# Optimization experiments

Measured on AMD Instinct MI355X. Metric: run time of the kernel, lower is better.

Reference implementation:

```python
import jax, jax.numpy as jnp
import numpy as np

N_NODES = 100000
N_EDGES = 3200000
NUM_FEATURES = 5
HIDDEN = 64


def _gcn_layer(x, W, b, src, dst, norm, n_nodes):
    """One GCNConv: out = scatter_add(norm * (xW)[src] -> dst) + b.
    src/dst/norm already include self-loops and symmetric normalization."""
    h = x @ W                                  # [N, out_ch] small dense GEMM
    msg = h[src] * norm[:, None]               # [E+N, out_ch] gather + scale
    out = jax.ops.segment_sum(msg, dst, num_segments=n_nodes)
    return out + b


def _build_norm(edge_index, n_nodes):
    """Add self-loops, compute D^{-1/2}[src] * D^{-1/2}[dst] (GCN symmetric norm)."""
    loop = jnp.arange(n_nodes, dtype=edge_index.dtype)
    src = jnp.concatenate([edge_index[0], loop])
    dst = jnp.concatenate([edge_index[1], loop])
    deg = jax.ops.segment_sum(jnp.ones_like(dst, dtype=jnp.float32), dst,
                              num_segments=n_nodes)
    dis = jnp.where(deg > 0, jax.lax.rsqrt(deg), 0.0)  # deg^{-1/2}
    norm = dis[src] * dis[dst]
    return src, dst, norm


def setup_inputs() -> dict:
    key = jax.random.key(0)
    ks = jax.random.split(key, 8)
    x = jax.random.normal(ks[0], (N_NODES, NUM_FEATURES), dtype=jnp.float32)
    edge_index = jax.random.randint(ks[1], (2, N_EDGES), 0, N_NODES, dtype=jnp.int64)
    # glorot-ish scaled params
    W1 = jax.random.normal(ks[2], (NUM_FEATURES, HIDDEN), dtype=jnp.float32) * (1.0 / np.sqrt(NUM_FEATURES))
    b1 = jnp.zeros((HIDDEN,), dtype=jnp.float32)
    W2 = jax.random.normal(ks[3], (HIDDEN, HIDDEN), dtype=jnp.float32) * (1.0 / np.sqrt(HIDDEN))
    b2 = jnp.zeros((HIDDEN,), dtype=jnp.float32)
    W3 = jax.random.normal(ks[4], (HIDDEN, 1), dtype=jnp.float32) * (1.0 / np.sqrt(HIDDEN))
    b3 = jnp.zeros((1,), dtype=jnp.float32)
    return {"x": x, "edge_index": edge_index,
            "W1": W1, "b1": b1, "W2": W2, "b2": b2, "W3": W3, "b3": b3}


def reference(x, edge_index, W1, b1, W2, b2, W3, b3):
    n_nodes = x.shape[0]
    src, dst, norm = _build_norm(edge_index, n_nodes)
    h = jax.nn.relu(_gcn_layer(x, W1, b1, src, dst, norm, n_nodes))
    h = jax.nn.relu(_gcn_layer(h, W2, b2, src, dst, norm, n_nodes))
    out = _gcn_layer(h, W3, b3, src, dst, norm, n_nodes)  # [N, 1]
    return out
```

## Files before the change

kernel.cpp:

```cpp
#include <hip/hip_runtime.h>
#include <hip/hip_fp16.h>

#define NFEAT 5
#define HID 64
#define BSH 9
#define BNODES 512
#define MAXBK 256
#define CHUNK 4096
#define ECAPMAX 20480

__global__ void k_binit(int* bcur, int ecap) {
    bcur[threadIdx.x] = threadIdx.x * ecap;
}

__global__ __launch_bounds__(256) void
k_bin(const int* __restrict__ src, const int* __restrict__ dst,
      int* bcur, unsigned* __restrict__ binned, int E) {
    __shared__ unsigned stg[CHUNK];
    __shared__ unsigned char bkt[CHUNK];
    __shared__ int hist[MAXBK], base[MAXBK], gb[MAXBK];
    int t = threadIdx.x;
    int e0 = blockIdx.x * CHUNK;
    int cc = E - e0; if (cc > CHUNK) cc = CHUNK;
    hist[t] = 0;
    __syncthreads();
    unsigned me[CHUNK / 256]; int mb[CHUNK / 256]; int mr[CHUNK / 256];
#pragma unroll
    for (int k = 0; k < CHUNK / 256; ++k) {
        int i = e0 + k * 256 + t;
        if (i < E) {
            int s = src[i], d = dst[i];
            mb[k] = d >> BSH;
            me[k] = (unsigned)s | ((unsigned)(d & (BNODES - 1)) << 17);
            mr[k] = atomicAdd(&hist[mb[k]], 1);
        } else mb[k] = -1;
    }
    __syncthreads();
    int c = hist[t];
    base[t] = c;
    __syncthreads();
    for (int off = 1; off < 256; off <<= 1) {
        int a = (t >= off) ? base[t - off] : 0;
        __syncthreads();
        base[t] += a;
        __syncthreads();
    }
    base[t] -= c;
    gb[t] = c ? atomicAdd(&bcur[t], c) : 0;
    __syncthreads();
#pragma unroll
    for (int k = 0; k < CHUNK / 256; ++k)
        if (mb[k] >= 0) {
            int p = base[mb[k]] + mr[k];
            stg[p] = me[k];
            bkt[p] = (unsigned char)mb[k];
        }
    __syncthreads();
#pragma unroll
    for (int k = 0; k < CHUNK / 256; ++k) {
        int p = k * 256 + t;
        if (p < cc) {
            int b = bkt[p];
            binned[gb[b] + (p - base[b])] = stg[p];
        }
    }
}

__global__ __launch_bounds__(256) void
k_sort(const unsigned* __restrict__ binned, const int* __restrict__ bcur,
       const float* __restrict__ x, int* __restrict__ rpN, int* __restrict__ rpE,
       int* __restrict__ csr, float* __restrict__ dis, float* __restrict__ xs,
       int n, int ecap) {
    __shared__ unsigned short rank[ECAPMAX];
    __shared__ int hist[BNODES];
    __shared__ int cur[BNODES];
    __shared__ int tmp[256];
    int t = threadIdx.x, b = blockIdx.x;
    int e0 = b * ecap;
    int cnt = bcur[b] - e0;
    if (cnt > ecap) cnt = ecap;
    int v0 = b << BSH;
    int nv = n - v0; if (nv > BNODES) nv = BNODES;
    hist[t] = 0; hist[t + 256] = 0;
    __syncthreads();
    for (int i = t; i < cnt; i += 256) {
        int vl = binned[e0 + i] >> 17;
        rank[i] = (unsigned short)atomicAdd(&hist[vl], 1);
    }
    __syncthreads();
    for (int vl = t; vl < nv; vl += 256) {
        int v = v0 + vl;
        float dv = rsqrtf((float)hist[vl] + 1.0f);
        dis[v] = dv;
        const float* xr = x + (size_t)v * NFEAT;
        float* xw = xs + (size_t)v * 8;
        xw[0] = dv * xr[0]; xw[1] = dv * xr[1]; xw[2] = dv * xr[2];
        xw[3] = dv * xr[3]; xw[4] = dv * xr[4];
        xw[5] = 0.f; xw[6] = 0.f; xw[7] = 0.f;
    }
    int b0 = t * 2;
    int c0 = hist[b0], c1 = hist[b0 + 1];
    int s = c0 + c1;
    tmp[t] = s;
    __syncthreads();
    for (int off = 1; off < 256; off <<= 1) {
        int a = (t >= off) ? tmp[t - off] : 0;
        __syncthreads();
        tmp[t] += a;
        __syncthreads();
    }
    int excl = e0 + tmp[t] - s;
    cur[b0] = excl;
    cur[b0 + 1] = excl + c0;
    if (b0 < nv)     { rpN[v0 + b0]     = excl;      rpE[v0 + b0]     = excl + c0; }
    if (b0 + 1 < nv) { rpN[v0 + b0 + 1] = excl + c0; rpE[v0 + b0 + 1] = excl + c0 + c1; }
    __syncthreads();
    for (int i = t; i < cnt; i += 256) {
        unsigned e = binned[e0 + i];
        int vl = e >> 17;
        csr[cur[vl] + rank[i]] = (int)(e & 0x1FFFF);
    }
}

__global__ __launch_bounds__(256) void
k_layer1(const int* __restrict__ rpN, const int* __restrict__ rpE,
         const int* __restrict__ csr, const float* __restrict__ xs,
         const float* __restrict__ dis, const float* __restrict__ W1,
         const float* __restrict__ b1, __half* __restrict__ g1h, int n) {
    int wave = (blockIdx.x * blockDim.x + threadIdx.x) >> 6;
    int lane = threadIdx.x & 63;
    if (wave >= n) return;
    int v = wave;
    int r0 = rpN[v], r1 = rpE[v];
    float a0 = 0.f, a1 = 0.f, a2 = 0.f, a3 = 0.f, a4 = 0.f;
    for (int j = r0 + lane; j < r1; j += 64) {
        const float4* q = (const float4*)(xs + (size_t)csr[j] * 8);
        float4 qa = q[0], qb = q[1];
        a0 += qa.x; a1 += qa.y; a2 += qa.z; a3 += qa.w; a4 += qb.x;
    }
#pragma unroll
    for (int m = 32; m > 0; m >>= 1) {
        a0 += __shfl_xor(a0, m, 64); a1 += __shfl_xor(a1, m, 64);
        a2 += __shfl_xor(a2, m, 64); a3 += __shfl_xor(a3, m, 64);
        a4 += __shfl_xor(a4, m, 64);
    }
    float dv = dis[v];
    const float* pv = xs + (size_t)v * 8;
    a0 = dv * (a0 + pv[0]); a1 = dv * (a1 + pv[1]); a2 = dv * (a2 + pv[2]);
    a3 = dv * (a3 + pv[3]); a4 = dv * (a4 + pv[4]);
    int c = lane;
    float h = b1[c] + a0 * W1[c] + a1 * W1[64 + c] + a2 * W1[128 + c]
            + a3 * W1[192 + c] + a4 * W1[256 + c];
    g1h[(size_t)v * HID + c] = __float2half(dv * fmaxf(h, 0.0f));
}

__global__ __launch_bounds__(256) void
k_layer23(const int* __restrict__ rpN, const int* __restrict__ rpE,
          const int* __restrict__ csr, const __half* __restrict__ g1h,
          const float* __restrict__ dis, const float* __restrict__ W2,
          const float* __restrict__ b2, const float* __restrict__ W3,
          float* __restrict__ svs, int n) {
    __shared__ float W2s[HID * HID];
    for (int i = threadIdx.x; i < HID * HID; i += 256) W2s[i] = W2[i];
    __syncthreads();
    int wave = (blockIdx.x * blockDim.x + threadIdx.x) >> 6;
    int lane = threadIdx.x & 63;
    if (wave >= n) return;
    int v = wave;
    int r0 = rpN[v], r1 = rpE[v];
    float acc = __half2float(g1h[(size_t)v * HID + lane]);
    int j = r0;
    for (; j + 8 <= r1; j += 8) {
        int s0 = csr[j],     s1 = csr[j + 1], s2 = csr[j + 2], s3 = csr[j + 3];
        int s4 = csr[j + 4], s5 = csr[j + 5], s6 = csr[j + 6], s7 = csr[j + 7];
        float t0 = __half2float(g1h[(size_t)s0 * HID + lane]);
        float t1 = __half2float(g1h[(size_t)s1 * HID + lane]);
        float t2 = __half2float(g1h[(size_t)s2 * HID + lane]);
        float t3 = __half2float(g1h[(size_t)s3 * HID + lane]);
        float t4 = __half2float(g1h[(size_t)s4 * HID + lane]);
        float t5 = __half2float(g1h[(size_t)s5 * HID + lane]);
        float t6 = __half2float(g1h[(size_t)s6 * HID + lane]);
        float t7 = __half2float(g1h[(size_t)s7 * HID + lane]);
        acc += ((t0 + t1) + (t2 + t3)) + ((t4 + t5) + (t6 + t7));
    }
    for (; j < r1; ++j) acc += __half2float(g1h[(size_t)csr[j] * HID + lane]);
    float dv = dis[v];
    acc *= dv;
    float out = b2[lane];
#pragma unroll
    for (int k = 0; k < HID; ++k)
        out = fmaf(__shfl(acc, k, 64), W2s[(k << 6) + lane], out);
    out = fmaxf(out, 0.0f);
    float val = out * W3[lane];
#pragma unroll
    for (int m = 32; m > 0; m >>= 1) val += __shfl_xor(val, m, 64);
    if (lane == 0) svs[v] = dv * val;
}

__global__ __launch_bounds__(256) void
k_out(const int* __restrict__ rpN, const int* __restrict__ rpE,
      const int* __restrict__ csr, const float* __restrict__ svs,
      const float* __restrict__ dis, const float* __restrict__ b3,
      float* __restrict__ out, int n) {
    int wave = (blockIdx.x * blockDim.x + threadIdx.x) >> 6;
    int lane = threadIdx.x & 63;
    if (wave >= n) return;
    int v = wave;
    int r0 = rpN[v], r1 = rpE[v];
    float acc = (lane == 0) ? svs[v] : 0.f;
    for (int j = r0 + lane; j < r1; j += 64) acc += svs[csr[j]];
#pragma unroll
    for (int m = 32; m > 0; m >>= 1) acc += __shfl_xor(acc, m, 64);
    if (lane == 0) out[v] = b3[0] + dis[v] * acc;
}

extern "C" void kernel_launch(void* const* d_in, const int* in_sizes, int n_in,
                              void* d_out, int out_size, void* d_ws, size_t ws_size,
                              hipStream_t stream) {
    const float* x  = (const float*)d_in[0];
    const int*   ei = (const int*)d_in[1];
    const float* W1 = (const float*)d_in[2];
    const float* b1 = (const float*)d_in[3];
    const float* W2 = (const float*)d_in[4];
    const float* b2 = (const float*)d_in[5];
    const float* W3 = (const float*)d_in[6];
    const float* b3 = (const float*)d_in[7];
    float* out = (float*)d_out;

    const int n = out_size;
    const int E = in_sizes[1] / 2;
    const int* src = ei;
    const int* dst = ei + E;

    const int nbk = (n + BNODES - 1) / BNODES;
    int ecap = E / nbk;
    ecap += ecap / 8 + 1024;
    if (ecap > ECAPMAX) ecap = ECAPMAX;

    int*      bcur   = (int*)d_ws;
    int*      rpN    = bcur + 512;
    int*      rpE    = rpN + n;
    float*    dis    = (float*)(rpE + n);
    float*    svs    = dis + n;
    int*      csr    = (int*)(svs + n);
    unsigned* binned = (unsigned*)(csr + (size_t)nbk * ecap);
    float*    xs     = (float*)(binned + (size_t)nbk * ecap);
    __half*   g1h    = (__half*)binned;

    const int B = 256;
    const int nchunk = (E + CHUNK - 1) / CHUNK;
    const int gridW  = ((size_t)n * 64 + B - 1) / B;

    k_binit  <<<1, 256, 0, stream>>>(bcur, ecap);
    k_bin    <<<nchunk, 256, 0, stream>>>(src, dst, bcur, binned, E);
    k_sort   <<<nbk, 256, 0, stream>>>(binned, bcur, x, rpN, rpE, csr, dis, xs, n, ecap);
    k_layer1 <<<gridW, B, 0, stream>>>(rpN, rpE, csr, xs, dis, W1, b1, g1h, n);
    k_layer23<<<gridW, B, 0, stream>>>(rpN, rpE, csr, g1h, dis, W2, b2, W3, svs, n);
    k_out    <<<gridW, B, 0, stream>>>(rpN, rpE, csr, svs, dis, b3, out, n);
}
```

Measured before the change: 371.7 us.

## Halve node bucket size, vectorize edge binning loads, enlarge layer23 blocks

```diff
diff --git a/kernel.cpp b/kernel.cpp
--- a/kernel.cpp
+++ b/kernel.cpp
@@ -3,11 +3,11 @@
 
 #define NFEAT 5
 #define HID 64
-#define BSH 9
-#define BNODES 512
-#define MAXBK 256
+#define BSH 8
+#define BNODES 256
+#define NBK2 512
 #define CHUNK 4096
-#define ECAPMAX 20480
+#define ECAPMAX 12288
 
 __global__ void k_binit(int* bcur, int ecap) {
     bcur[threadIdx.x] = threadIdx.x * ecap;
@@ -17,47 +17,76 @@
 k_bin(const int* __restrict__ src, const int* __restrict__ dst,
       int* bcur, unsigned* __restrict__ binned, int E) {
     __shared__ unsigned stg[CHUNK];
-    __shared__ unsigned char bkt[CHUNK];
-    __shared__ int hist[MAXBK], base[MAXBK], gb[MAXBK];
+    __shared__ unsigned short bkt[CHUNK];
+    __shared__ int hist[NBK2], base[NBK2], gb[NBK2];
+    __shared__ int tmp[256];
     int t = threadIdx.x;
     int e0 = blockIdx.x * CHUNK;
     int cc = E - e0; if (cc > CHUNK) cc = CHUNK;
-    hist[t] = 0;
-    __syncthreads();
-    unsigned me[CHUNK / 256]; int mb[CHUNK / 256]; int mr[CHUNK / 256];
-#pragma unroll
-    for (int k = 0; k < CHUNK / 256; ++k) {
-        int i = e0 + k * 256 + t;
-        if (i < E) {
-            int s = src[i], d = dst[i];
-            mb[k] = d >> BSH;
-            me[k] = (unsigned)s | ((unsigned)(d & (BNODES - 1)) << 17);
-            mr[k] = atomicAdd(&hist[mb[k]], 1);
-        } else mb[k] = -1;
-    }
-    __syncthreads();
-    int c = hist[t];
-    base[t] = c;
+    hist[t] = 0; hist[t + 256] = 0;
+    __syncthreads();
+    unsigned me[16]; int mb[16]; unsigned short mr[16];
+    const int4* src4 = (const int4*)(src + e0);
+    const int4* dst4 = (const int4*)(dst + e0);
+#pragma unroll
+    for (int k = 0; k < 4; ++k) {
+        int i4 = k * 256 + t;
+        int ib = i4 * 4;
+        int ss[4], dd[4];
+        bool any = false;
+        if (e0 + ib + 3 < E) {
+            int4 s4 = src4[i4], d4 = dst4[i4];
+            ss[0]=s4.x; ss[1]=s4.y; ss[2]=s4.z; ss[3]=s4.w;
+            dd[0]=d4.x; dd[1]=d4.y; dd[2]=d4.z; dd[3]=d4.w;
+            any = true;
+#pragma unroll
+            for (int j = 0; j < 4; ++j) mb[k*4+j] = 0;
+        } else {
+#pragma unroll
+            for (int j = 0; j < 4; ++j) {
+                if (e0 + ib + j < E) { ss[j]=src[e0+ib+j]; dd[j]=dst[e0+ib+j]; any=true; mb[k*4+j]=0; }
+                else mb[k*4+j] = -1;
+            }
+        }
+        if (any) {
+#pragma unroll
+            for (int j = 0; j < 4; ++j) {
+                int idx = k * 4 + j;
+                if (mb[idx] >= 0) {
+                    mb[idx] = dd[j] >> BSH;
+                    me[idx] = (unsigned)ss[j] | ((unsigned)(dd[j] & (BNODES - 1)) << 17);
+                    mr[idx] = (unsigned short)atomicAdd(&hist[mb[idx]], 1);
+                }
+            }
+        }
+    }
+    __syncthreads();
+    int c0 = hist[2*t], c1 = hist[2*t + 1];
+    int s = c0 + c1;
+    tmp[t] = s;
     __syncthreads();
     for (int off = 1; off < 256; off <<= 1) {
-        int a = (t >= off) ? base[t - off] : 0;
-        __syncthreads();
-        base[t] += a;
-        __syncthreads();
-    }
-    base[t] -= c;
-    gb[t] = c ? atomicAdd(&bcur[t], c) : 0;
-    __syncthreads();
-#pragma unroll
-    for (int k = 0; k < CHUNK / 256; ++k)
+        int a = (t >= off) ? tmp[t - off] : 0;
+        __syncthreads();
+        tmp[t] += a;
+        __syncthreads();
+    }
+    int excl = tmp[t] - s;
+    base[2*t]     = excl;
+    base[2*t + 1] = excl + c0;
+    gb[2*t]     = c0 ? atomicAdd(&bcur[2*t], c0) : 0;
+    gb[2*t + 1] = c1 ? atomicAdd(&bcur[2*t + 1], c1) : 0;
+    __syncthreads();
+#pragma unroll
+    for (int k = 0; k < 16; ++k)
         if (mb[k] >= 0) {
             int p = base[mb[k]] + mr[k];
             stg[p] = me[k];
-            bkt[p] = (unsigned char)mb[k];
-        }
-    __syncthreads();
-#pragma unroll
-    for (int k = 0; k < CHUNK / 256; ++k) {
+            bkt[p] = (unsigned short)mb[k];
+        }
+    __syncthreads();
+#pragma unroll
+    for (int k = 0; k < 16; ++k) {
         int p = k * 256 + t;
         if (p < cc) {
             int b = bkt[p];
@@ -81,16 +110,16 @@
     if (cnt > ecap) cnt = ecap;
     int v0 = b << BSH;
     int nv = n - v0; if (nv > BNODES) nv = BNODES;
-    hist[t] = 0; hist[t + 256] = 0;
+    hist[t] = 0;
     __syncthreads();
     for (int i = t; i < cnt; i += 256) {
         int vl = binned[e0 + i] >> 17;
         rank[i] = (unsigned short)atomicAdd(&hist[vl], 1);
     }
     __syncthreads();
-    for (int vl = t; vl < nv; vl += 256) {
-        int v = v0 + vl;
-        float dv = rsqrtf((float)hist[vl] + 1.0f);
+    if (t < nv) {
+        int v = v0 + t;
+        float dv = rsqrtf((float)hist[t] + 1.0f);
         dis[v] = dv;
         const float* xr = x + (size_t)v * NFEAT;
         float* xw = xs + (size_t)v * 8;
@@ -98,10 +127,8 @@
         xw[3] = dv * xr[3]; xw[4] = dv * xr[4];
         xw[5] = 0.f; xw[6] = 0.f; xw[7] = 0.f;
     }
-    int b0 = t * 2;
-    int c0 = hist[b0], c1 = hist[b0 + 1];
-    int s = c0 + c1;
-    tmp[t] = s;
+    int c = hist[t];
+    tmp[t] = c;
     __syncthreads();
     for (int off = 1; off < 256; off <<= 1) {
         int a = (t >= off) ? tmp[t - off] : 0;
@@ -109,11 +136,9 @@
         tmp[t] += a;
         __syncthreads();
     }
-    int excl = e0 + tmp[t] - s;
-    cur[b0] = excl;
-    cur[b0 + 1] = excl + c0;
-    if (b0 < nv)     { rpN[v0 + b0]     = excl;      rpE[v0 + b0]     = excl + c0; }
-    if (b0 + 1 < nv) { rpN[v0 + b0 + 1] = excl + c0; rpE[v0 + b0 + 1] = excl + c0 + c1; }
+    int excl = e0 + tmp[t] - c;
+    cur[t] = excl;
+    if (t < nv) { rpN[v0 + t] = excl; rpE[v0 + t] = excl + c; }
     __syncthreads();
     for (int i = t; i < cnt; i += 256) {
         unsigned e = binned[e0 + i];
@@ -154,14 +179,14 @@
     g1h[(size_t)v * HID + c] = __float2half(dv * fmaxf(h, 0.0f));
 }
 
-__global__ __launch_bounds__(256) void
+__global__ __launch_bounds__(1024) void
 k_layer23(const int* __restrict__ rpN, const int* __restrict__ rpE,
           const int* __restrict__ csr, const __half* __restrict__ g1h,
           const float* __restrict__ dis, const float* __restrict__ W2,
           const float* __restrict__ b2, const float* __restrict__ W3,
           float* __restrict__ svs, int n) {
     __shared__ float W2s[HID * HID];
-    for (int i = threadIdx.x; i < HID * HID; i += 256) W2s[i] = W2[i];
+    for (int i = threadIdx.x; i < HID * HID; i += 1024) W2s[i] = W2[i];
     __syncthreads();
     int wave = (blockIdx.x * blockDim.x + threadIdx.x) >> 6;
     int lane = threadIdx.x & 63;
@@ -250,11 +275,12 @@
     const int B = 256;
     const int nchunk = (E + CHUNK - 1) / CHUNK;
     const int gridW  = ((size_t)n * 64 + B - 1) / B;
-
-    k_binit  <<<1, 256, 0, stream>>>(bcur, ecap);
+    const int grid23 = ((size_t)n * 64 + 1023) / 1024;
+
+    k_binit  <<<1, 512, 0, stream>>>(bcur, ecap);
     k_bin    <<<nchunk, 256, 0, stream>>>(src, dst, bcur, binned, E);
     k_sort   <<<nbk, 256, 0, stream>>>(binned, bcur, x, rpN, rpE, csr, dis, xs, n, ecap);
     k_layer1 <<<gridW, B, 0, stream>>>(rpN, rpE, csr, xs, dis, W1, b1, g1h, n);
-    k_layer23<<<gridW, B, 0, stream>>>(rpN, rpE, csr, g1h, dis, W2, b2, W3, svs, n);
+    k_layer23<<<grid23, 1024, 0, stream>>>(rpN, rpE, csr, g1h, dis, W2, b2, W3, svs, n);
     k_out    <<<gridW, B, 0, stream>>>(rpN, rpE, csr, svs, dis, b3, out, n);
 }
```

Result: no change. 367.3 us (-1.2%).
